# Performance work log

Measured on AMD Instinct MI355X. Metric: run time of the kernel, lower is better.

## Reference

```python
import jax, jax.numpy as jnp
import numpy as np

N, M, IN, H, OUT, L = 100000, 50000, 256, 256, 128, 2
E_RAND = 150000  # extra random incidences beyond coverage prefixes
GN_STRUCT_EPS = float(H)  # GraphNorm(hidden, hidden): 2nd positional arg is eps!


def _l2n(a):
    return a / jnp.maximum(jnp.linalg.norm(a, axis=1, keepdims=True), 1e-12)


def _ln(x, g, b, eps=1e-5):
    m = x.mean(-1, keepdims=True)
    v = ((x - m) ** 2).mean(-1, keepdims=True)
    return (x - m) / jnp.sqrt(v + eps) * g + b


def _gn(x, w, b, ms, eps):
    # PyG GraphNorm with batch=None (single graph)
    mean = x.mean(0, keepdims=True)
    out = x - mean * ms
    var = (out ** 2).mean(0, keepdims=True)
    return w * out / jnp.sqrt(var + eps) + b


def _hgconv(xn, W, bias, src, dst, n_nodes, n_edges):
    # PyG HypergraphConv, use_attention=False -> heads=1, lin has no bias
    xw = xn @ W.T                                                # [n_nodes, H]
    ones = jnp.ones(src.shape[0], xw.dtype)
    Dn = jax.ops.segment_sum(ones, src, num_segments=n_nodes)   # node degree
    Dn = jnp.where(Dn > 0, 1.0 / Dn, 0.0)
    Be = jax.ops.segment_sum(ones, dst, num_segments=n_edges)   # hyperedge degree
    Be = jnp.where(Be > 0, 1.0 / Be, 0.0)
    he = jax.ops.segment_sum(xw[src], dst, num_segments=n_edges) * Be[:, None]
    out = jax.ops.segment_sum(he[dst], src, num_segments=n_nodes) * Dn[:, None]
    return out + bias


def _forward(x, x_e, x_struct_table, w_in, b_in, w_e, b_e, w_sem, b_sem,
             ln_n_g, ln_n_b, hg_w, hg_b,
             gn_struct_w, gn_struct_b, gn_struct_ms,
             gn_llm_w, gn_llm_b, gn_llm_ms,
             gn_d_w, gn_d_b, gn_d_ms,
             skip_w, skip_b,
             nf_ln1_g, nf_ln1_b, nf_w, nf_b, nf_ln2_g, nf_ln2_b,
             ef_ln1_g, ef_ln1_b, ef_w, ef_b, ef_ln2_g, ef_ln2_b,
             lin_w, lin_b, edge_index):
    lrelu = jax.nn.leaky_relu  # slope 0.01 == nn.LeakyReLU default
    src, dst = edge_index[0], edge_index[1]
    n, m = x.shape[0], x_e.shape[0]
    # edge_index[0] covers all nodes, so unique(edge_index[0]) == arange(N)
    xs = lrelu(_l2n(x_struct_table) @ w_in.T + b_in)   # dropout: eval mode (identity)
    xn = lrelu(_l2n(x) @ w_sem.T + b_sem)
    xe = lrelu(_l2n(x_e) @ w_e.T + b_e)
    for i in range(L):
        xs = _ln(xs, ln_n_g[i], ln_n_b[i])
        xs = lrelu(_hgconv(xs, hg_w[i, 0], hg_b[i, 0], src, dst, n, m)) + \
             _gn(xs, gn_struct_w[i], gn_struct_b[i], gn_struct_ms[i], GN_STRUCT_EPS)
        xn = _gn(xn, gn_llm_w[i], gn_llm_b[i], gn_llm_ms[i], 1e-5)
        xn = lrelu(_hgconv(xn, hg_w[i, 1], hg_b[i, 1], src, dst, n, m)) + \
             (xn @ skip_w[i, 0].T + skip_b[i, 0])
        agg = jax.ops.segment_min(xn[src], dst, num_segments=m)  # MinAggregation
        xe = _gn(xe + agg, gn_d_w[i], gn_d_b[i], gn_d_ms[i], 1e-5)
        # dual hypergraph: hyperedges become nodes (flip of edge_index)
        xe = lrelu(_hgconv(xe, hg_w[i, 2], hg_b[i, 2], dst, src, m, n)) + \
             (xe @ skip_w[i, 1].T + skip_b[i, 1])
    xf = jnp.concatenate([xs, xn], axis=1)
    xf = _ln(xf, nf_ln1_g, nf_ln1_b)
    xf = lrelu(xf @ nf_w.T + nf_b)
    xf = _ln(xf, nf_ln2_g, nf_ln2_b)
    xa = jax.ops.segment_min(xf[src], dst, num_segments=m)
    xef = jnp.concatenate([xa, xe], axis=1)
    xef = _ln(xef, ef_ln1_g, ef_ln1_b)
    xef = lrelu(xef @ ef_w.T + ef_b)
    xef = _ln(xef, ef_ln2_g, ef_ln2_b)
    return xef @ lin_w.T + lin_b  # [M, OUT]


def setup_inputs() -> dict:
    key = jax.random.key(0)
    ks = iter(jax.random.split(key, 64))
    def nrm(shape, scale=0.05):
        return jax.random.normal(next(ks), shape, dtype=jnp.float32) * scale
    # incidence list with guaranteed coverage of all nodes and all hyperedges
    src = jnp.concatenate([jnp.arange(N),
                           jax.random.randint(next(ks), (M + E_RAND,), 0, N)])
    dst = jnp.concatenate([jax.random.randint(next(ks), (N,), 0, M),
                           jnp.arange(M),
                           jax.random.randint(next(ks), (E_RAND,), 0, M)])
    edge_index = jnp.stack([src, dst]).astype(jnp.int32)  # [2, 300000]
    return dict(
        x=nrm((N, IN), 1.0), x_e=nrm((M, IN), 1.0), x_struct_table=nrm((N, IN), 1.0),
        w_in=nrm((H, IN)), b_in=jnp.zeros((H,)),
        w_e=nrm((H, IN)), b_e=jnp.zeros((H,)),
        w_sem=nrm((H, IN)), b_sem=jnp.zeros((H,)),
        ln_n_g=jnp.ones((L, H)), ln_n_b=jnp.zeros((L, H)),
        hg_w=nrm((L, 3, H, H)), hg_b=jnp.zeros((L, 3, H)),
        gn_struct_w=jnp.ones((L, H)), gn_struct_b=jnp.zeros((L, H)), gn_struct_ms=jnp.ones((L, H)),
        gn_llm_w=jnp.ones((L, H)), gn_llm_b=jnp.zeros((L, H)), gn_llm_ms=jnp.ones((L, H)),
        gn_d_w=jnp.ones((L, H)), gn_d_b=jnp.zeros((L, H)), gn_d_ms=jnp.ones((L, H)),
        skip_w=nrm((L, 2, H, H)), skip_b=jnp.zeros((L, 2, H)),
        nf_ln1_g=jnp.ones((2 * H,)), nf_ln1_b=jnp.zeros((2 * H,)),
        nf_w=nrm((H, 2 * H)), nf_b=jnp.zeros((H,)),
        nf_ln2_g=jnp.ones((H,)), nf_ln2_b=jnp.zeros((H,)),
        ef_ln1_g=jnp.ones((2 * H,)), ef_ln1_b=jnp.zeros((2 * H,)),
        ef_w=nrm((H, 2 * H)), ef_b=jnp.zeros((H,)),
        ef_ln2_g=jnp.ones((H,)), ef_ln2_b=jnp.zeros((H,)),
        lin_w=nrm((OUT, H)), lin_b=jnp.zeros((OUT,)),
        edge_index=edge_index,
    )


def reference(x, x_e, x_struct_table, w_in, b_in, w_e, b_e, w_sem, b_sem,
              ln_n_g, ln_n_b, hg_w, hg_b,
              gn_struct_w, gn_struct_b, gn_struct_ms,
              gn_llm_w, gn_llm_b, gn_llm_ms,
              gn_d_w, gn_d_b, gn_d_ms,
              skip_w, skip_b,
              nf_ln1_g, nf_ln1_b, nf_w, nf_b, nf_ln2_g, nf_ln2_b,
              ef_ln1_g, ef_ln1_b, ef_w, ef_b, ef_ln2_g, ef_ln2_b,
              lin_w, lin_b, edge_index):
    return _forward(x, x_e, x_struct_table, w_in, b_in, w_e, b_e, w_sem, b_sem,
                    ln_n_g, ln_n_b, hg_w, hg_b,
                    gn_struct_w, gn_struct_b, gn_struct_ms,
                    gn_llm_w, gn_llm_b, gn_llm_ms,
                    gn_d_w, gn_d_b, gn_d_ms,
                    skip_w, skip_b,
                    nf_ln1_g, nf_ln1_b, nf_w, nf_b, nf_ln2_g, nf_ln2_b,
                    ef_ln1_g, ef_ln1_b, ef_w, ef_b, ef_ln2_g, ef_ln2_b,
                    lin_w, lin_b, edge_index)
```

## Files before the change

kernel.cpp:

```cpp
#include <hip/hip_runtime.h>

typedef unsigned short u16;
struct __align__(16) us8 { ushort4 a, b; };
typedef __attribute__((ext_vector_type(8))) short bf16x8;
typedef __attribute__((ext_vector_type(4))) float f32x4;

#define CDIV(a,b) (((a)+(b)-1)/(b))

__device__ __forceinline__ float bf2f(u16 u){ return __uint_as_float(((unsigned)u)<<16); }
__device__ __forceinline__ u16 f2bf(float f){
  unsigned u=__float_as_uint(f);
  unsigned r=u+0x7fffu+((u>>16)&1u);
  return (u16)(r>>16);
}
__device__ __forceinline__ float lrelu_f(float v){ return v>0.f? v:0.01f*v; }
__device__ __forceinline__ float wsum(float v){
  #pragma unroll
  for(int o=32;o>0;o>>=1) v+=__shfl_xor(v,o,64);
  return v;
}
__device__ __forceinline__ void us8_to_f(const us8& v, float* f){
  f[0]=bf2f(v.a.x); f[1]=bf2f(v.a.y); f[2]=bf2f(v.a.z); f[3]=bf2f(v.a.w);
  f[4]=bf2f(v.b.x); f[5]=bf2f(v.b.y); f[6]=bf2f(v.b.z); f[7]=bf2f(v.b.w);
}
__device__ __forceinline__ us8 f_to_us8(const float* f){
  us8 v;
  v.a.x=f2bf(f[0]); v.a.y=f2bf(f[1]); v.a.z=f2bf(f[2]); v.a.w=f2bf(f[3]);
  v.b.x=f2bf(f[4]); v.b.y=f2bf(f[5]); v.b.z=f2bf(f[6]); v.b.w=f2bf(f[7]);
  return v;
}

__global__ void zero_k(unsigned* __restrict__ p, int n){
  int i=blockIdx.x*256+threadIdx.x; if(i<n) p[i]=0u;
}
__global__ void cvt_k(const float* __restrict__ in, u16* __restrict__ out, int n){
  int i = (blockIdx.x*256+threadIdx.x)*4;
  if(i+3<n){
    float4 v=*(const float4*)(in+i);
    ushort4 o; o.x=f2bf(v.x); o.y=f2bf(v.y); o.z=f2bf(v.z); o.w=f2bf(v.w);
    *(ushort4*)(out+i)=o;
  } else {
    for(int q=0;q<4&&i+q<n;q++) out[i+q]=f2bf(in[i+q]);
  }
}

__global__ void count_k(const int* __restrict__ src, const int* __restrict__ dst, int E,
                        int* __restrict__ cnt_src, int* __restrict__ cnt_dst){
  int e = blockIdx.x*256+threadIdx.x;
  if(e>=E) return;
  atomicAdd(&cnt_src[src[e]],1);
  atomicAdd(&cnt_dst[dst[e]],1);
}

#define SCAN_CHUNK 1024
__global__ void scan_pass1(const int* __restrict__ in, int n, int* __restrict__ partial){
  __shared__ int red[256];
  int base = blockIdx.x*SCAN_CHUNK;
  int s=0;
  for(int j=threadIdx.x;j<SCAN_CHUNK;j+=256){ int i=base+j; if(i<n) s+=in[i]; }
  red[threadIdx.x]=s; __syncthreads();
  for(int st=128;st>0;st>>=1){ if(threadIdx.x<st) red[threadIdx.x]+=red[threadIdx.x+st]; __syncthreads(); }
  if(threadIdx.x==0) partial[blockIdx.x]=red[0];
}
__global__ void scan_pass2(int* __restrict__ partial, int nb){
  __shared__ int buf[1024];
  for(int j=threadIdx.x;j<1024;j+=256) buf[j] = (j<nb)? partial[j]:0;
  __syncthreads();
  if(threadIdx.x==0){ int run=0; for(int j=0;j<nb;j++){ int v=buf[j]; buf[j]=run; run+=v; } }
  __syncthreads();
  for(int j=threadIdx.x;j<nb;j+=256) partial[j]=buf[j];
}
__global__ void scan_pass3(const int* __restrict__ in, int n, const int* __restrict__ partial,
                           int* __restrict__ out, int total){
  __shared__ int red[256];
  int base = blockIdx.x*SCAN_CHUNK;
  int j0 = base + threadIdx.x*4;
  int v[4]; int s=0;
  #pragma unroll
  for(int q=0;q<4;q++){ int i=j0+q; v[q]=(i<n)? in[i]:0; s+=v[q]; }
  red[threadIdx.x]=s; __syncthreads();
  if(threadIdx.x==0){ int run=0; for(int j=0;j<256;j++){ int t=red[j]; red[j]=run; run+=t; } }
  __syncthreads();
  int run = partial[blockIdx.x] + red[threadIdx.x];
  #pragma unroll
  for(int q=0;q<4;q++){ int i=j0+q; if(i<n) out[i]=run; run+=v[q]; }
  if(base==0 && threadIdx.x==0) out[n]=total;
}
__global__ void copy_int_k(const int* __restrict__ in, int* __restrict__ out, int n){
  int i=blockIdx.x*256+threadIdx.x;
  if(i<n) out[i]=in[i];
}
__global__ void fill_adj_k(const int* __restrict__ src, const int* __restrict__ dst, int E,
                           int* __restrict__ cur_src, int* __restrict__ cur_dst,
                           int* __restrict__ adj_sd, int* __restrict__ adj_ds){
  int e = blockIdx.x*256+threadIdx.x;
  if(e>=E) return;
  int s=src[e], d=dst[e];
  int p = atomicAdd(&cur_dst[d],1); adj_ds[p]=s;
  int q = atomicAdd(&cur_src[s],1); adj_sd[q]=d;
}
__global__ void invdeg_k(const int* __restrict__ off, float* __restrict__ inv, int S){
  int s=blockIdx.x*256+threadIdx.x;
  if(s>=S) return;
  int d=off[s+1]-off[s];
  inv[s] = d>0 ? 1.0f/(float)d : 0.0f;
}

__global__ void l2norm_k(const float* __restrict__ in, u16* __restrict__ out, int R){
  int r = blockIdx.x*4 + (threadIdx.x>>6);
  if(r>=R) return;
  int c = (threadIdx.x&63)*4;
  float4 v = *(const float4*)(in + (size_t)r*256 + c);
  float q = wsum(v.x*v.x+v.y*v.y+v.z*v.z+v.w*v.w);
  float sc = 1.0f/fmaxf(sqrtf(q),1e-12f);
  ushort4 o; o.x=f2bf(v.x*sc); o.y=f2bf(v.y*sc); o.z=f2bf(v.z*sc); o.w=f2bf(v.w*sc);
  *(ushort4*)(out + (size_t)r*256 + c) = o;
}

__global__ void ln_rows_k(u16* __restrict__ x, const float* __restrict__ g,
                          const float* __restrict__ b, int R){
  int r = blockIdx.x*4 + (threadIdx.x>>6);
  if(r>=R) return;
  int lane = threadIdx.x&63; int c = lane*4;
  u16* row = x + (size_t)r*256;
  ushort4 u = *(const ushort4*)(row + c);
  float v0=bf2f(u.x), v1=bf2f(u.y), v2=bf2f(u.z), v3=bf2f(u.w);
  float mean = wsum(v0+v1+v2+v3) * (1.f/256.f);
  float d0=v0-mean,d1=v1-mean,d2=v2-mean,d3=v3-mean;
  float var = wsum(d0*d0+d1*d1+d2*d2+d3*d3) * (1.f/256.f);
  float inv = 1.0f/sqrtf(var + 1e-5f);
  ushort4 ov;
  ov.x=f2bf(d0*inv*g[c+0]+b[c+0]);
  ov.y=f2bf(d1*inv*g[c+1]+b[c+1]);
  ov.z=f2bf(d2*inv*g[c+2]+b[c+2]);
  ov.w=f2bf(d3*inv*g[c+3]+b[c+3]);
  *(ushort4*)(row + c) = ov;
}

__global__ void ln512_k(u16* __restrict__ Lb, u16* __restrict__ Rb,
                        const float* __restrict__ g, const float* __restrict__ b, int R){
  int r = blockIdx.x*4 + (threadIdx.x>>6);
  if(r>=R) return;
  int lane = threadIdx.x&63; int c = lane*4;
  u16* rowL = Lb + (size_t)r*256;
  u16* rowR = Rb + (size_t)r*256;
  ushort4 ul = *(const ushort4*)(rowL + c);
  ushort4 ur = *(const ushort4*)(rowR + c);
  float l0=bf2f(ul.x), l1=bf2f(ul.y), l2=bf2f(ul.z), l3=bf2f(ul.w);
  float r0=bf2f(ur.x), r1=bf2f(ur.y), r2=bf2f(ur.z), r3=bf2f(ur.w);
  float mean = wsum(l0+l1+l2+l3+r0+r1+r2+r3) * (1.f/512.f);
  float a0=l0-mean,a1=l1-mean,a2=l2-mean,a3=l3-mean;
  float b0=r0-mean,b1=r1-mean,b2=r2-mean,b3=r3-mean;
  float var = wsum(a0*a0+a1*a1+a2*a2+a3*a3+b0*b0+b1*b1+b2*b2+b3*b3) * (1.f/512.f);
  float inv = 1.0f/sqrtf(var + 1e-5f);
  int cr = 256+c;
  ushort4 ovl, ovr;
  ovl.x=f2bf(a0*inv*g[c+0]+b[c+0]);
  ovl.y=f2bf(a1*inv*g[c+1]+b[c+1]);
  ovl.z=f2bf(a2*inv*g[c+2]+b[c+2]);
  ovl.w=f2bf(a3*inv*g[c+3]+b[c+3]);
  ovr.x=f2bf(b0*inv*g[cr+0]+b[cr+0]);
  ovr.y=f2bf(b1*inv*g[cr+1]+b[cr+1]);
  ovr.z=f2bf(b2*inv*g[cr+2]+b[cr+2]);
  ovr.w=f2bf(b3*inv*g[cr+3]+b[cr+3]);
  *(ushort4*)(rowL + c) = ovl;
  *(ushort4*)(rowR + c) = ovr;
}

__global__ void colstat_k(const u16* __restrict__ x, const u16* __restrict__ x2,
                          float* __restrict__ stat, int R){
  __shared__ float sh[512];
  int tid = threadIdx.x;
  for(int j=tid;j<512;j+=256) sh[j]=0.f;
  __syncthreads();
  int c = (tid&63)*4;
  float s0=0,s1=0,s2=0,s3=0,q0=0,q1=0,q2=0,q3=0;
  for(int r=blockIdx.x*4+(tid>>6); r<R; r+=gridDim.x*4){
    ushort4 u = *(const ushort4*)(x + (size_t)r*256 + c);
    float v0=bf2f(u.x), v1=bf2f(u.y), v2=bf2f(u.z), v3=bf2f(u.w);
    if(x2){
      ushort4 w = *(const ushort4*)(x2 + (size_t)r*256 + c);
      v0+=bf2f(w.x); v1+=bf2f(w.y); v2+=bf2f(w.z); v3+=bf2f(w.w);
    }
    s0+=v0; s1+=v1; s2+=v2; s3+=v3;
    q0+=v0*v0; q1+=v1*v1; q2+=v2*v2; q3+=v3*v3;
  }
  atomicAdd(&sh[c+0],s0); atomicAdd(&sh[c+1],s1);
  atomicAdd(&sh[c+2],s2); atomicAdd(&sh[c+3],s3);
  atomicAdd(&sh[256+c+0],q0); atomicAdd(&sh[256+c+1],q1);
  atomicAdd(&sh[256+c+2],q2); atomicAdd(&sh[256+c+3],q3);
  __syncthreads();
  for(int j=tid;j<512;j+=256) atomicAdd(&stat[j], sh[j]);
}
__global__ void gn_final_k(const float* __restrict__ stat, const float* __restrict__ w,
                           const float* __restrict__ b, const float* __restrict__ ms,
                           float eps, float invR,
                           float* __restrict__ gA, float* __restrict__ gS, float* __restrict__ gB){
  int c=threadIdx.x;
  float mean = stat[c]*invR;
  float a = mean*ms[c];
  float ex2 = stat[256+c]*invR;
  float var = ex2 - 2.f*a*mean + a*a;
  gA[c]=a;
  gS[c]=w[c]/sqrtf(var+eps);
  gB[c]=b[c];
}
__global__ void apply_gn_k(u16* __restrict__ x, const u16* __restrict__ add,
                           const float* __restrict__ gA, const float* __restrict__ gS,
                           const float* __restrict__ gB, size_t n4){
  size_t stride = (size_t)gridDim.x*256;
  for(size_t p=(size_t)blockIdx.x*256+threadIdx.x; p<n4; p+=stride){
    int c = (int)(p&63)*4;
    ushort4 u = ((const ushort4*)x)[p];
    float v0=bf2f(u.x), v1=bf2f(u.y), v2=bf2f(u.z), v3=bf2f(u.w);
    if(add){
      ushort4 a = ((const ushort4*)add)[p];
      v0+=bf2f(a.x); v1+=bf2f(a.y); v2+=bf2f(a.z); v3+=bf2f(a.w);
    }
    v0 = fmaf(gS[c+0], v0-gA[c+0], gB[c+0]);
    v1 = fmaf(gS[c+1], v1-gA[c+1], gB[c+1]);
    v2 = fmaf(gS[c+2], v2-gA[c+2], gB[c+2]);
    v3 = fmaf(gS[c+3], v3-gA[c+3], gB[c+3]);
    ushort4 o; o.x=f2bf(v0); o.y=f2bf(v1); o.z=f2bf(v2); o.w=f2bf(v3);
    ((ushort4*)x)[p]=o;
  }
}

template<int MODE>
__global__ void seg_sum_k(const u16* __restrict__ in, u16* __restrict__ out,
    const int* __restrict__ adj, const int* __restrict__ off,
    const float* __restrict__ inv, const float* __restrict__ bias,
    const u16* __restrict__ resid,
    const float* __restrict__ gA, const float* __restrict__ gS, const float* __restrict__ gB,
    int S){
  int s = blockIdx.x*8 + (threadIdx.x>>5);
  if(s>=S) return;
  int c = (threadIdx.x&31)*8;
  int jb=off[s], je=off[s+1];
  float a[8]={0.f,0.f,0.f,0.f,0.f,0.f,0.f,0.f};
  for(int j=jb;j<je;j++){
    us8 v = *(const us8*)(in + (size_t)adj[j]*256 + c);
    float f[8]; us8_to_f(v,f);
    #pragma unroll
    for(int q=0;q<8;q++) a[q]+=f[q];
  }
  float sc = inv[s];
  float o[8];
  if(MODE==0){
    #pragma unroll
    for(int q=0;q<8;q++) o[q]=a[q]*sc;
  } else {
    #pragma unroll
    for(int q=0;q<8;q++) o[q] = lrelu_f(fmaf(a[q],sc,bias[c+q]));
    us8 p = *(const us8*)(resid + (size_t)s*256 + c);
    float pf[8]; us8_to_f(p,pf);
    if(MODE==1){
      #pragma unroll
      for(int q=0;q<8;q++) o[q] += fmaf(gS[c+q], pf[q]-gA[c+q], gB[c+q]);
    } else {
      #pragma unroll
      for(int q=0;q<8;q++) o[q] += pf[q];
    }
  }
  *(us8*)(out + (size_t)s*256 + c) = f_to_us8(o);
}

__global__ void seg_min_k(const u16* __restrict__ in, u16* __restrict__ out,
    const int* __restrict__ adj, const int* __restrict__ off, int S){
  int s = blockIdx.x*8 + (threadIdx.x>>5);
  if(s>=S) return;
  int c = (threadIdx.x&31)*8;
  int jb=off[s], je=off[s+1];
  float m[8];
  #pragma unroll
  for(int q=0;q<8;q++) m[q]=3.402823466e38f;
  for(int j=jb;j<je;j++){
    us8 v = *(const us8*)(in + (size_t)adj[j]*256 + c);
    float f[8]; us8_to_f(v,f);
    #pragma unroll
    for(int q=0;q<8;q++) m[q]=fminf(m[q],f[q]);
  }
  if(jb==je){
    #pragma unroll
    for(int q=0;q<8;q++) m[q]=0.f;
  }
  *(us8*)(out + (size_t)s*256 + c) = f_to_us8(m);
}

template<int FLAGS, int JT>
__global__ __launch_bounds__(512, 4)
void gemm_mfma(const u16* A0, const u16* __restrict__ A1,
               const u16* __restrict__ Wb, const float* __restrict__ bias,
               u16* Cb, float* __restrict__ Cf, int R, int K){
  const int CN = JT*64;
  __shared__ u16 sm[(128+256)*72];
  u16* As = sm;
  u16* Bs = sm + 128*72;
  const int t = threadIdx.x;
  const int row0 = blockIdx.x*128;
  const int lane = t&63;
  const int w = t>>6;
  const int wrow = (w>>2)*64, wcol = (w&3)*(JT*16);
  const int lm = lane&15, q = lane>>4;
  const int ar = t>>3, ac = (t&7)*8;
  f32x4 acc[4][4];
  #pragma unroll
  for(int i=0;i<4;i++)
    #pragma unroll
    for(int j=0;j<JT;j++) acc[i][j] = (f32x4){0.f,0.f,0.f,0.f};

  us8 av[2], bv[4];
  auto load_tile = [&](int kt){
    const u16* Ab = ((FLAGS&8) && kt>=256) ? A1 : A0;
    const int kloc = kt & 255;
    #pragma unroll
    for(int p=0;p<2;p++){
      int rg = row0 + p*64 + ar;
      if(rg<R) av[p] = *(const us8*)(Ab + (size_t)rg*256 + kloc + ac);
      else { av[p].a=make_ushort4(0,0,0,0); av[p].b=av[p].a; }
    }
    #pragma unroll
    for(int p=0;p<JT;p++)
      bv[p] = *(const us8*)(Wb + (size_t)(p*64 + ar)*K + kt + ac);
  };

  load_tile(0);
  for(int kt=0; kt<K; kt+=64){
    #pragma unroll
    for(int p=0;p<2;p++) *(us8*)(&As[(p*64+ar)*72+ac]) = av[p];
    #pragma unroll
    for(int p=0;p<JT;p++) *(us8*)(&Bs[(p*64+ar)*72+ac]) = bv[p];
    __syncthreads();
    if(kt+64<K) load_tile(kt+64);
    #pragma unroll
    for(int ks=0; ks<2; ks++){
      const int ko = ks*32 + q*8;
      bf16x8 af[4], bfv[4];
      #pragma unroll
      for(int i=0;i<4;i++) af[i]  = *(const bf16x8*)(&As[(wrow + i*16 + lm)*72 + ko]);
      #pragma unroll
      for(int j=0;j<JT;j++) bfv[j] = *(const bf16x8*)(&Bs[(wcol + j*16 + lm)*72 + ko]);
      #pragma unroll
      for(int i=0;i<4;i++)
        #pragma unroll
        for(int j=0;j<JT;j++)
          acc[i][j] = __builtin_amdgcn_mfma_f32_16x16x32_bf16(af[i], bfv[j], acc[i][j], 0,0,0);
    }
    __syncthreads();
  }

  float bvals[4];
  #pragma unroll
  for(int j=0;j<JT;j++) bvals[j] = (FLAGS&1) ? bias[wcol+j*16+lm] : 0.f;

  if(FLAGS&4){
    #pragma unroll
    for(int j=0;j<JT;j++){
      int col = wcol + j*16 + lm;
      #pragma unroll
      for(int i=0;i<4;i++){
        int rbase = row0 + wrow + i*16 + q*4;
        #pragma unroll
        for(int rg=0;rg<4;rg++){
          int r = rbase+rg;
          if(r>=R) continue;
          float v = acc[i][j][rg] + bvals[j];
          if(FLAGS&2) v = lrelu_f(v);
          Cf[(size_t)r*CN+col] = v;
        }
      }
    }
  } else {
    const int CEPI = CN+8;
    const int ROWU = CN/8;
    #pragma unroll
    for(int h=0; h<2; h++){
      if((w>>2)==h){
        #pragma unroll
        for(int j=0;j<JT;j++){
          int cl = wcol + j*16 + lm;
          #pragma unroll
          for(int i=0;i<4;i++){
            #pragma unroll
            for(int rg=0;rg<4;rg++){
              float v = acc[i][j][rg] + bvals[j];
              if(FLAGS&2) v = lrelu_f(v);
              sm[(i*16 + q*4 + rg)*CEPI + cl] = f2bf(v);
            }
          }
        }
      }
      __syncthreads();
      #pragma unroll
      for(int it=0; it<64*ROWU/512; it++){
        int idx = it*512 + t;
        int rl = idx/ROWU, c8 = (idx - rl*ROWU)*8;
        int r = row0 + h*64 + rl;
        if(r<R) *(us8*)(Cb + (size_t)r*CN + c8) = *(const us8*)(&sm[rl*CEPI + c8]);
      }
      __syncthreads();
    }
  }
}

extern "C" void kernel_launch(void* const* d_in, const int* in_sizes, int n_in,
                              void* d_out, int out_size, void* d_ws, size_t ws_size,
                              hipStream_t stream){
  const int H = 256;
  const int N = in_sizes[0]/H;
  const int M = in_sizes[1]/H;
  const int E = in_sizes[38]/2;

  const float* x     = (const float*)d_in[0];
  const float* x_e   = (const float*)d_in[1];
  const float* x_st  = (const float*)d_in[2];
  const float* w_in  = (const float*)d_in[3];  const float* b_in  = (const float*)d_in[4];
  const float* w_e   = (const float*)d_in[5];  const float* b_e   = (const float*)d_in[6];
  const float* w_sem = (const float*)d_in[7];  const float* b_sem = (const float*)d_in[8];
  const float* ln_n_g = (const float*)d_in[9]; const float* ln_n_b = (const float*)d_in[10];
  const float* hg_w  = (const float*)d_in[11]; const float* hg_b  = (const float*)d_in[12];
  const float* gns_w = (const float*)d_in[13]; const float* gns_b = (const float*)d_in[14]; const float* gns_ms = (const float*)d_in[15];
  const float* gnl_w = (const float*)d_in[16]; const float* gnl_b = (const float*)d_in[17]; const float* gnl_ms = (const float*)d_in[18];
  const float* gnd_w = (const float*)d_in[19]; const float* gnd_b = (const float*)d_in[20]; const float* gnd_ms = (const float*)d_in[21];
  const float* skip_w = (const float*)d_in[22]; const float* skip_b = (const float*)d_in[23];
  const float* nf_ln1_g = (const float*)d_in[24]; const float* nf_ln1_b = (const float*)d_in[25];
  const float* nf_w = (const float*)d_in[26]; const float* nf_b = (const float*)d_in[27];
  const float* nf_ln2_g = (const float*)d_in[28]; const float* nf_ln2_b = (const float*)d_in[29];
  const float* ef_ln1_g = (const float*)d_in[30]; const float* ef_ln1_b = (const float*)d_in[31];
  const float* ef_w = (const float*)d_in[32]; const float* ef_b = (const float*)d_in[33];
  const float* ef_ln2_g = (const float*)d_in[34]; const float* ef_ln2_b = (const float*)d_in[35];
  const float* lin_w = (const float*)d_in[36]; const float* lin_b = (const float*)d_in[37];
  const int* edge = (const int*)d_in[38];
  const int* src = edge;
  const int* dst = edge + E;
  float* outp = (float*)d_out;

  const size_t NH=(size_t)N*H, MH=(size_t)M*H;
  u16* XS = (u16*)d_ws;
  u16* XN = XS + NH;
  u16* TN = XN + NH;
  u16* XE = TN + NH;
  u16* TM = XE + MH;
  float* dinv = (float*)(TM + MH);
  float* binv = dinv + N;
  float* stat = binv + M;
  float* gA = stat+512; float* gS = gA+256; float* gB = gS+256;
  int* cnt_src = (int*)(gB+256);
  int* cnt_dst = cnt_src + N;
  int* off_src = cnt_dst + M;
  int* off_dst = off_src + (N+1);
  int* adj_ds = off_dst + (M+1);
  int* adj_sd = adj_ds + E;
  int* partial = adj_sd + E;
  u16* wb = (u16*)(((uintptr_t)(partial+1024)+15)&~(uintptr_t)15);
  u16* wb_in  = wb;
  u16* wb_sem = wb_in  + 65536;
  u16* wb_e   = wb_sem + 65536;
  u16* wb_hg  = wb_e   + 65536;
  u16* wb_sk  = wb_hg  + 6*65536;
  u16* wb_nf  = wb_sk  + 4*65536;
  u16* wb_ef  = wb_nf  + 131072;
  u16* wb_lin = wb_ef  + 131072;

  cvt_k<<<CDIV(65536,1024),256,0,stream>>>(w_in, wb_in, 65536);
  cvt_k<<<CDIV(65536,1024),256,0,stream>>>(w_sem, wb_sem, 65536);
  cvt_k<<<CDIV(65536,1024),256,0,stream>>>(w_e, wb_e, 65536);
  cvt_k<<<CDIV(6*65536,1024),256,0,stream>>>(hg_w, wb_hg, 6*65536);
  cvt_k<<<CDIV(4*65536,1024),256,0,stream>>>(skip_w, wb_sk, 4*65536);
  cvt_k<<<CDIV(131072,1024),256,0,stream>>>(nf_w, wb_nf, 131072);
  cvt_k<<<CDIV(131072,1024),256,0,stream>>>(ef_w, wb_ef, 131072);
  cvt_k<<<CDIV(32768,1024),256,0,stream>>>(lin_w, wb_lin, 32768);

  zero_k<<<CDIV(N+M,256),256,0,stream>>>((unsigned*)cnt_src, N+M);
  count_k<<<CDIV(E,256),256,0,stream>>>(src,dst,E,cnt_src,cnt_dst);
  int nbN = CDIV(N,SCAN_CHUNK), nbM = CDIV(M,SCAN_CHUNK);
  scan_pass1<<<nbN,256,0,stream>>>(cnt_src,N,partial);
  scan_pass2<<<1,256,0,stream>>>(partial,nbN);
  scan_pass3<<<nbN,256,0,stream>>>(cnt_src,N,partial,off_src,E);
  scan_pass1<<<nbM,256,0,stream>>>(cnt_dst,M,partial);
  scan_pass2<<<1,256,0,stream>>>(partial,nbM);
  scan_pass3<<<nbM,256,0,stream>>>(cnt_dst,M,partial,off_dst,E);
  copy_int_k<<<CDIV(N,256),256,0,stream>>>(off_src,cnt_src,N);
  copy_int_k<<<CDIV(M,256),256,0,stream>>>(off_dst,cnt_dst,M);
  fill_adj_k<<<CDIV(E,256),256,0,stream>>>(src,dst,E,cnt_src,cnt_dst,adj_sd,adj_ds);
  invdeg_k<<<CDIV(N,256),256,0,stream>>>(off_src,dinv,N);
  invdeg_k<<<CDIV(M,256),256,0,stream>>>(off_dst,binv,M);

  auto gemm = [&](int F, const u16* A0, const u16* A1, const u16* Wt, const float* bias,
                  u16* Cb, float* Cf, int R, int K){
    dim3 g(CDIV(R,128));
    switch(F){
      case 0:  gemm_mfma<0,4> <<<g,512,0,stream>>>(A0,A1,Wt,bias,Cb,Cf,R,K); break;
      case 1:  gemm_mfma<1,4> <<<g,512,0,stream>>>(A0,A1,Wt,bias,Cb,Cf,R,K); break;
      case 3:  gemm_mfma<3,4> <<<g,512,0,stream>>>(A0,A1,Wt,bias,Cb,Cf,R,K); break;
      case 5:  gemm_mfma<5,2> <<<g,512,0,stream>>>(A0,A1,Wt,bias,Cb,Cf,R,K); break;
      case 11: gemm_mfma<11,4><<<g,512,0,stream>>>(A0,A1,Wt,bias,Cb,Cf,R,K); break;
    }
  };
  auto colstats = [&](const u16* xx, const u16* x2, const float* w, const float* b,
                      const float* ms, float eps, int R){
    zero_k<<<2,256,0,stream>>>((unsigned*)stat, 512);
    colstat_k<<<256,256,0,stream>>>(xx, x2, stat, R);
    gn_final_k<<<1,256,0,stream>>>(stat, w, b, ms, eps, 1.0f/(float)R, gA,gS,gB);
  };

  l2norm_k<<<CDIV(N,4),256,0,stream>>>(x_st, TN, N);
  gemm(3, TN, nullptr, wb_in, b_in, XS, nullptr, N, 256);
  l2norm_k<<<CDIV(N,4),256,0,stream>>>(x, TN, N);
  gemm(3, TN, nullptr, wb_sem, b_sem, XN, nullptr, N, 256);
  l2norm_k<<<CDIV(M,4),256,0,stream>>>(x_e, TM, M);
  gemm(3, TM, nullptr, wb_e, b_e, XE, nullptr, M, 256);

  for(int i=0;i<2;i++){
    ln_rows_k<<<CDIV(N,4),256,0,stream>>>(XS, ln_n_g+i*H, ln_n_b+i*H, N);
    colstats(XS, nullptr, gns_w+i*H, gns_b+i*H, gns_ms+i*H, 256.0f, N);
    seg_sum_k<0><<<CDIV(M,8),256,0,stream>>>(XS, TM, adj_ds, off_dst, binv, nullptr,nullptr,nullptr,nullptr,nullptr, M);
    gemm(0, TM, nullptr, wb_hg+(size_t)(i*3+0)*65536, nullptr, TM, nullptr, M, 256);
    seg_sum_k<1><<<CDIV(N,8),256,0,stream>>>(TM, XS, adj_sd, off_src, dinv, hg_b+(size_t)(i*3+0)*H, XS, gA,gS,gB, N);

    colstats(XN, nullptr, gnl_w+i*H, gnl_b+i*H, gnl_ms+i*H, 1e-5f, N);
    apply_gn_k<<<1024,256,0,stream>>>(XN, nullptr, gA,gS,gB, NH/4);
    seg_sum_k<0><<<CDIV(M,8),256,0,stream>>>(XN, TM, adj_ds, off_dst, binv, nullptr,nullptr,nullptr,nullptr,nullptr, M);
    gemm(0, TM, nullptr, wb_hg+(size_t)(i*3+1)*65536, nullptr, TM, nullptr, M, 256);
    gemm(1, XN, nullptr, wb_sk+(size_t)(i*2+0)*65536, skip_b+(size_t)(i*2+0)*H, TN, nullptr, N, 256);
    seg_sum_k<2><<<CDIV(N,8),256,0,stream>>>(TM, XN, adj_sd, off_src, dinv, hg_b+(size_t)(i*3+1)*H, TN, nullptr,nullptr,nullptr, N);

    seg_min_k<<<CDIV(M,8),256,0,stream>>>(XN, TM, adj_ds, off_dst, M);
    colstats(XE, TM, gnd_w+i*H, gnd_b+i*H, gnd_ms+i*H, 1e-5f, M);
    apply_gn_k<<<1024,256,0,stream>>>(XE, TM, gA,gS,gB, MH/4);
    gemm(0, XE, nullptr, wb_hg+(size_t)(i*3+2)*65536, nullptr, TM, nullptr, M, 256);
    seg_sum_k<0><<<CDIV(N,8),256,0,stream>>>(TM, TN, adj_sd, off_src, dinv, nullptr,nullptr,nullptr,nullptr,nullptr, N);
    gemm(1, XE, nullptr, wb_sk+(size_t)(i*2+1)*65536, skip_b+(size_t)(i*2+1)*H, TM, nullptr, M, 256);
    seg_sum_k<2><<<CDIV(M,8),256,0,stream>>>(TN, XE, adj_ds, off_dst, binv, hg_b+(size_t)(i*3+2)*H, TM, nullptr,nullptr,nullptr, M);
  }

  ln512_k<<<CDIV(N,4),256,0,stream>>>(XS, XN, nf_ln1_g, nf_ln1_b, N);
  gemm(11, XS, XN, wb_nf, nf_b, TN, nullptr, N, 512);
  ln_rows_k<<<CDIV(N,4),256,0,stream>>>(TN, nf_ln2_g, nf_ln2_b, N);
  seg_min_k<<<CDIV(M,8),256,0,stream>>>(TN, TM, adj_ds, off_dst, M);
  ln512_k<<<CDIV(M,4),256,0,stream>>>(TM, XE, ef_ln1_g, ef_ln1_b, M);
  gemm(11, TM, XE, wb_ef, ef_b, XS, nullptr, M, 512);
  ln_rows_k<<<CDIV(M,4),256,0,stream>>>(XS, ef_ln2_g, ef_ln2_b, M);
  gemm(5, XS, nullptr, wb_lin, lin_b, nullptr, outp, M, 256);
}
```

Measured before the change: 2.070 ms.

## Load GEMM MFMA operands directly from global memory, dropping LDS staging

The MFMA GEMM no longer stages A and W tiles through shared memory with barriers. Each wave now reads its bf16x8 fragments straight from global memory (relying on L1/L2 for reuse), iterating K in steps of 32 with unroll 2. Out-of-range rows are clamped to the last valid row instead of being zero-filled. Launch bounds drop to 3 blocks per CU to leave more registers. This removes __syncthreads and LDS traffic, but adds redundant global loads across waves plus uncoalesced 16-byte row accesses. The smaller shared array is kept, presumably for the epilogue.

```diff
diff --git a/kernel.cpp b/kernel.cpp
--- a/kernel.cpp
+++ b/kernel.cpp
@@ -288,65 +288,48 @@
 }
 
 template<int FLAGS, int JT>
-__global__ __launch_bounds__(512, 4)
+__global__ __launch_bounds__(512, 3)
 void gemm_mfma(const u16* A0, const u16* __restrict__ A1,
                const u16* __restrict__ Wb, const float* __restrict__ bias,
                u16* Cb, float* __restrict__ Cf, int R, int K){
   const int CN = JT*64;
-  __shared__ u16 sm[(128+256)*72];
-  u16* As = sm;
-  u16* Bs = sm + 128*72;
+  __shared__ u16 sm[64*(JT*64+8)];
   const int t = threadIdx.x;
   const int row0 = blockIdx.x*128;
   const int lane = t&63;
   const int w = t>>6;
   const int wrow = (w>>2)*64, wcol = (w&3)*(JT*16);
   const int lm = lane&15, q = lane>>4;
-  const int ar = t>>3, ac = (t&7)*8;
   f32x4 acc[4][4];
   #pragma unroll
   for(int i=0;i<4;i++)
     #pragma unroll
     for(int j=0;j<JT;j++) acc[i][j] = (f32x4){0.f,0.f,0.f,0.f};
 
-  us8 av[2], bv[4];
-  auto load_tile = [&](int kt){
+  int arow[4];
+  #pragma unroll
+  for(int i=0;i<4;i++){
+    int r = row0 + wrow + i*16 + lm;
+    arow[i] = r < R ? r : (R-1);
+  }
+  const u16* brow[JT];
+  #pragma unroll
+  for(int j=0;j<JT;j++) brow[j] = Wb + (size_t)(wcol + j*16 + lm)*K + q*8;
+
+  #pragma unroll 2
+  for(int kt=0; kt<K; kt+=32){
     const u16* Ab = ((FLAGS&8) && kt>=256) ? A1 : A0;
-    const int kloc = kt & 255;
-    #pragma unroll
-    for(int p=0;p<2;p++){
-      int rg = row0 + p*64 + ar;
-      if(rg<R) av[p] = *(const us8*)(Ab + (size_t)rg*256 + kloc + ac);
-      else { av[p].a=make_ushort4(0,0,0,0); av[p].b=av[p].a; }
-    }
-    #pragma unroll
-    for(int p=0;p<JT;p++)
-      bv[p] = *(const us8*)(Wb + (size_t)(p*64 + ar)*K + kt + ac);
-  };
-
-  load_tile(0);
-  for(int kt=0; kt<K; kt+=64){
-    #pragma unroll
-    for(int p=0;p<2;p++) *(us8*)(&As[(p*64+ar)*72+ac]) = av[p];
-    #pragma unroll
-    for(int p=0;p<JT;p++) *(us8*)(&Bs[(p*64+ar)*72+ac]) = bv[p];
-    __syncthreads();
-    if(kt+64<K) load_tile(kt+64);
-    #pragma unroll
-    for(int ks=0; ks<2; ks++){
-      const int ko = ks*32 + q*8;
-      bf16x8 af[4], bfv[4];
+    const int kc = (kt & 255) + q*8;
+    bf16x8 af[4], bfv[4];
+    #pragma unroll
+    for(int i=0;i<4;i++)  af[i]  = *(const bf16x8*)(Ab + (size_t)arow[i]*256 + kc);
+    #pragma unroll
+    for(int j=0;j<JT;j++) bfv[j] = *(const bf16x8*)(brow[j] + kt);
+    #pragma unroll
+    for(int i=0;i<4;i++)
       #pragma unroll
-      for(int i=0;i<4;i++) af[i]  = *(const bf16x8*)(&As[(wrow + i*16 + lm)*72 + ko]);
-      #pragma unroll
-      for(int j=0;j<JT;j++) bfv[j] = *(const bf16x8*)(&Bs[(wcol + j*16 + lm)*72 + ko]);
-      #pragma unroll
-      for(int i=0;i<4;i++)
-        #pragma unroll
-        for(int j=0;j<JT;j++)
-          acc[i][j] = __builtin_amdgcn_mfma_f32_16x16x32_bf16(af[i], bfv[j], acc[i][j], 0,0,0);
-    }
-    __syncthreads();
+      for(int j=0;j<JT;j++)
+        acc[i][j] = __builtin_amdgcn_mfma_f32_16x16x32_bf16(af[i], bfv[j], acc[i][j], 0,0,0);
   }
 
   float bvals[4];
```

Result: slower. 2.163 ms (+4.5%).
